# Optimization experiments

Hardware: AMD Instinct MI355X
Metric: run time of the kernel (lower is better)

The kernel has to match this reference:

```python
import jax, jax.numpy as jnp
import numpy as np

GRID = (52, 52)       # (grid_h, grid_w)
N_BOXES = 5
NORM = (416, 416)     # (norm_h, norm_w)
N_POLY = 4
IOU_THRESH = 0.4


def setup_inputs() -> dict:
    key = jax.random.key(0)
    x = jax.random.uniform(
        key, (1, GRID[0], GRID[1], N_BOXES * (N_POLY + 1)), dtype=jnp.float32)
    return {"x": x}


def _decode_coord(coord):
    # coord: [1, gh, gw, n_boxes, 4] -> decoded xyxy boxes [1, gh, gw, n_boxes, 4]
    gh, gw = GRID
    off_y, off_x = jnp.mgrid[:gh, :gw]
    off_x = off_x[None, :, :, None].astype(jnp.float32)   # [1, gh, gw, 1]
    off_y = off_y[None, :, :, None].astype(jnp.float32)
    sx = NORM[1] / gw
    sy = NORM[0] / gh
    cx = (coord[..., 0] + off_x) * sx
    w = coord[..., 2] * sx
    cy = (coord[..., 1] + off_y) * sy
    h = coord[..., 3] * sy
    cy = NORM[0] - cy  # y-axis flip as in original
    return jnp.stack([cx - w / 2, cy - h / 2, cx + w / 2, cy + h / 2], axis=-1)


def _nms_keep(boxes, scores):
    # Greedy NMS identical to tf.image.non_max_suppression (max_output = N).
    # Returns boolean keep mask in ORIGINAL box order.
    N = boxes.shape[0]
    order = jnp.argsort(-scores)           # descending by score
    b = boxes[order]
    x1, y1, x2, y2 = b[:, 0], b[:, 1], b[:, 2], b[:, 3]
    area = jnp.maximum(x2 - x1, 0.0) * jnp.maximum(y2 - y1, 0.0)
    iw = jnp.maximum(jnp.minimum(x2[:, None], x2[None, :]) -
                     jnp.maximum(x1[:, None], x1[None, :]), 0.0)
    ih = jnp.maximum(jnp.minimum(y2[:, None], y2[None, :]) -
                     jnp.maximum(y1[:, None], y1[None, :]), 0.0)
    inter = iw * ih
    union = area[:, None] + area[None, :] - inter
    iou = jnp.where(union > 0, inter / jnp.maximum(union, 1e-12), 0.0)  # [N, N]
    idx = jnp.arange(N)

    def body(i, active):
        suppress = (iou[i] > IOU_THRESH) & (idx > i) & active[i]
        return active & ~suppress

    active = jax.lax.fori_loop(0, N, body, jnp.ones(N, dtype=bool))
    return jnp.zeros(N, dtype=bool).at[order].set(active)


def reference(x):
    gh, gw = GRID
    y = x.reshape(1, gh, gw, N_BOXES, N_POLY + 1)
    boxes = _decode_coord(y[..., :4]).reshape(-1, 4)   # [N, 4]
    scores = y[..., 4].reshape(-1)                     # [N]
    keep = _nms_keep(jax.lax.stop_gradient(boxes),
                     jax.lax.stop_gradient(scores))
    # gather_nd + scatter_nd back into zeros == masked scores
    nms_scores = jnp.where(keep, scores, 0.0)
    out = jnp.concatenate([boxes[None], nms_scores[None, :, None]], axis=-1)
    return out.reshape(1, -1, N_POLY + 1)
```

## Files before the change

kernel.cpp:

```cpp
#include <hip/hip_runtime.h>

#define GH 52
#define GW 52
#define NB 5
#define NCELL (GH*GW)
#define NBOX (NCELL*NB)
#define SCALE 8.0f
#define NORMY 416.0f
#define IOU_T 0.4f

#define TS 4
#define HS (TS+2)
#define TBOX (HS*HS*NB)
#define NTX (GW/TS)
#define NTY (GH/TS)

#define PW (GW+2)
#define PCELLS ((GH+2)*PW)

__global__ __launch_bounds__(192) void decode_adj_kernel(
        const float* __restrict__ x, float* __restrict__ out,
        unsigned long long* __restrict__ masks) {
    __shared__ float4 lbox[TBOX];
    __shared__ float  lsc[TBOX];
    int bx0 = (blockIdx.x % NTX) * TS;
    int by0 = (blockIdx.x / NTX) * TS;
    int t = threadIdx.x;

    if (t < TBOX) {
        int lcell = t / NB, b = t % NB;
        int lx = lcell % HS, ly = lcell / HS;
        int gx = bx0 + lx - 1, gy = by0 + ly - 1;
        float4 bb = make_float4(0.f, 0.f, 0.f, 0.f);
        float s = -1e30f;
        if (gx >= 0 && gx < GW && gy >= 0 && gy < GH) {
            const float* p = x + ((size_t)(gy * GW + gx) * NB + b) * 5;
            float c0 = p[0], c1 = p[1], c2 = p[2], c3 = p[3]; s = p[4];
            float cx = (c0 + (float)gx) * SCALE;
            float w  = c2 * SCALE;
            float cy = NORMY - (c1 + (float)gy) * SCALE;
            float h  = c3 * SCALE;
            bb = make_float4(cx - w * 0.5f, cy - h * 0.5f,
                             cx + w * 0.5f, cy + h * 0.5f);
        }
        lbox[t] = bb; lsc[t] = s;
    }
    __syncthreads();

    if (t < TS * TS * NB) {
        int lcell = t / NB, b = t % NB;
        int lxi = lcell % TS, lyi = lcell / TS;
        int gx = bx0 + lxi, gy = by0 + lyi;
        int lt = ((lyi + 1) * HS + (lxi + 1)) * NB + b;
        float4 bj = lbox[lt]; float sj = lsc[lt];
        int cell = gy * GW + gx;
        int j = cell * NB + b;
        float areaj = fmaxf(bj.z - bj.x, 0.f) * fmaxf(bj.w - bj.y, 0.f);
        unsigned long long m = 0ull;
        #pragma unroll
        for (int dy = -1; dy <= 1; ++dy)
        #pragma unroll
        for (int dx = -1; dx <= 1; ++dx)
        #pragma unroll
        for (int nb2 = 0; nb2 < NB; ++nb2) {
            int ln = ((lyi + 1 + dy) * HS + (lxi + 1 + dx)) * NB + nb2;
            int i = j + (dy * GW + dx) * NB + (nb2 - b);
            if (i == j) continue;
            float si = lsc[ln];
            bool earlier = (si > sj) || (si == sj && i < j);
            if (!earlier) continue;
            float4 bi = lbox[ln];
            float iw = fmaxf(fminf(bi.z, bj.z) - fmaxf(bi.x, bj.x), 0.f);
            float ih = fmaxf(fminf(bi.w, bj.w) - fmaxf(bi.y, bj.y), 0.f);
            float inter = iw * ih;
            float areai = fmaxf(bi.z - bi.x, 0.f) * fmaxf(bi.w - bi.y, 0.f);
            float uni = areai + areaj - inter;
            float iou = (uni > 0.f) ? inter / fmaxf(uni, 1e-12f) : 0.f;
            if (iou > IOU_T)
                m |= 1ull << ((dy + 1) * 15 + (dx + 1) * 5 + nb2);
        }
        masks[b * NCELL + cell] = m;
        out[j * 5 + 0] = bj.x; out[j * 5 + 1] = bj.y;
        out[j * 5 + 2] = bj.z; out[j * 5 + 3] = bj.w;
        out[j * 5 + 4] = sj;
    }
}

__global__ __launch_bounds__(1024) void nms_kernel(
        const unsigned long long* __restrict__ masks,
        float* __restrict__ out) {
    __shared__ unsigned char act_s[PCELLS];
    __shared__ unsigned int rowflag[3][GH + 2];
    int tid = threadIdx.x;

    unsigned long long cm[3][NB];
    bool own[3];
    #pragma unroll
    for (int k = 0; k < 3; ++k) {
        int ct = tid + k * 1024;
        own[k] = (ct < NCELL);
        #pragma unroll
        for (int b = 0; b < NB; ++b)
            cm[k][b] = own[k] ? masks[b * NCELL + ct] : 0ull;
    }

    for (int i = tid; i < PCELLS; i += 1024) act_s[i] = 0;
    if (tid < GH + 2) {
        rowflag[0][tid] = 0;
        rowflag[1][tid] = 0;
        rowflag[2][tid] = (tid >= 1 && tid <= GH) ? 1u : 0u;
    }
    __syncthreads();
    for (int i = tid; i < NCELL; i += 1024) {
        int gy = i / GW, gx = i % GW;
        act_s[(gy + 1) * PW + (gx + 1)] = 0x1F;
    }
    __syncthreads();

    volatile unsigned char* act = act_s;

    int pprev = 2, pcur = 0, pnext = 1;
    for (int pass = 0; pass < 256; ++pass) {
        if (tid < GH + 2) rowflag[pnext][tid] = 0;
        const unsigned int* prevf = rowflag[pprev];
        bool mych = false;
        #pragma unroll
        for (int k = 0; k < 3; ++k) {
            if (!own[k]) continue;
            int ct = tid + k * 1024;
            int gy = ct / GW, gx = ct % GW;
            if ((prevf[gy] | prevf[gy + 1] | prevf[gy + 2]) == 0u) continue;
            int p0 = gy * PW + gx;
            unsigned r0 = (unsigned)act[p0]          | ((unsigned)act[p0 + 1] << 5)
                        | ((unsigned)act[p0 + 2] << 10);
            unsigned r1 = (unsigned)act[p0 + PW]     | ((unsigned)act[p0 + PW + 1] << 5)
                        | ((unsigned)act[p0 + PW + 2] << 10);
            unsigned r2 = (unsigned)act[p0 + 2 * PW] | ((unsigned)act[p0 + 2 * PW + 1] << 5)
                        | ((unsigned)act[p0 + 2 * PW + 2] << 10);
            unsigned long long V = (unsigned long long)r0
                                 | ((unsigned long long)r1 << 15)
                                 | ((unsigned long long)r2 << 30);
            unsigned nb = 0;
            #pragma unroll
            for (int b = 0; b < NB; ++b)
                nb |= ((V & cm[k][b]) == 0ull ? 1u : 0u) << b;
            int pc = p0 + PW + 1;
            if ((unsigned char)nb != act[pc]) {
                act[pc] = (unsigned char)nb;
                atomicOr(&rowflag[pcur][gy + 1], 1u);
                mych = true;
            }
        }
        if (__syncthreads_count(mych ? 1 : 0) == 0) break;
        int t0 = pprev; pprev = pcur; pcur = pnext; pnext = t0;
    }

    #pragma unroll
    for (int k = 0; k < 3; ++k) {
        if (!own[k]) continue;
        int ct = tid + k * 1024;
        int gy = ct / GW, gx = ct % GW;
        unsigned bits = act_s[(gy + 1) * PW + (gx + 1)];
        #pragma unroll
        for (int b = 0; b < NB; ++b) {
            int j = ct * NB + b;
            if (!((bits >> b) & 1u)) out[j * 5 + 4] = 0.0f;
        }
    }
}

extern "C" void kernel_launch(void* const* d_in, const int* in_sizes, int n_in,
                              void* d_out, int out_size, void* d_ws, size_t ws_size,
                              hipStream_t stream) {
    const float* x = (const float*)d_in[0];
    float* out = (float*)d_out;

    unsigned long long* masks = (unsigned long long*)d_ws;

    decode_adj_kernel<<<NTX * NTY, 192, 0, stream>>>(x, out, masks);
    nms_kernel<<<1, 1024, 0, stream>>>(masks, out);
}
```

Baseline: 72.26 us.

## Assign four-cell horizontal strips per thread in NMS fixed-point kernel

```diff
diff --git a/kernel.cpp b/kernel.cpp
--- a/kernel.cpp
+++ b/kernel.cpp
@@ -15,8 +15,12 @@
 #define NTX (GW/TS)
 #define NTY (GH/TS)
 
-#define PW (GW+2)
-#define PCELLS ((GH+2)*PW)
+#define PW2 56
+#define PR  54
+#define PC2 (PR*PW2)
+#define NSTRIP 13
+#define NTHR (GH*NSTRIP)
+#define BLK 704
 
 __global__ __launch_bounds__(192) void decode_adj_kernel(
         const float* __restrict__ x, float* __restrict__ out,
@@ -86,85 +90,90 @@
     }
 }
 
-__global__ __launch_bounds__(1024) void nms_kernel(
+__global__ __launch_bounds__(BLK) void nms_kernel(
         const unsigned long long* __restrict__ masks,
         float* __restrict__ out) {
-    __shared__ unsigned char act_s[PCELLS];
-    __shared__ unsigned int rowflag[3][GH + 2];
+    __shared__ __align__(16) unsigned char act_s[PC2];
+    __shared__ unsigned int rowflag[3][PR];
     int tid = threadIdx.x;
+    bool wk = tid < NTHR;
+    int row = tid / NSTRIP;
+    int s   = tid - row * NSTRIP;
+    int gx0 = s * 4;
+    int cell0 = row * GW + gx0;
 
-    unsigned long long cm[3][NB];
-    bool own[3];
+    unsigned long long cm[4][NB];
     #pragma unroll
-    for (int k = 0; k < 3; ++k) {
-        int ct = tid + k * 1024;
-        own[k] = (ct < NCELL);
+    for (int c = 0; c < 4; ++c)
         #pragma unroll
         for (int b = 0; b < NB; ++b)
-            cm[k][b] = own[k] ? masks[b * NCELL + ct] : 0ull;
-    }
+            cm[c][b] = wk ? masks[b * NCELL + cell0 + c] : 0ull;
 
-    for (int i = tid; i < PCELLS; i += 1024) act_s[i] = 0;
-    if (tid < GH + 2) {
+    for (int i = tid; i < PC2; i += BLK) act_s[i] = 0;
+    if (tid < PR) {
         rowflag[0][tid] = 0;
         rowflag[1][tid] = 0;
         rowflag[2][tid] = (tid >= 1 && tid <= GH) ? 1u : 0u;
     }
     __syncthreads();
-    for (int i = tid; i < NCELL; i += 1024) {
-        int gy = i / GW, gx = i % GW;
-        act_s[(gy + 1) * PW + (gx + 1)] = 0x1F;
+    for (int i = tid; i < NCELL; i += BLK) {
+        int gy = i / GW, gxx = i - gy * GW;
+        act_s[(gy + 1) * PW2 + gxx + 1] = 0x1F;
     }
     __syncthreads();
 
-    volatile unsigned char* act = act_s;
+    int p0 = row * PW2 + gx0;
+    int pc = (row + 1) * PW2 + gx0 + 1;
 
     int pprev = 2, pcur = 0, pnext = 1;
     for (int pass = 0; pass < 256; ++pass) {
-        if (tid < GH + 2) rowflag[pnext][tid] = 0;
+        if (tid < PR) rowflag[pnext][tid] = 0;
         const unsigned int* prevf = rowflag[pprev];
         bool mych = false;
-        #pragma unroll
-        for (int k = 0; k < 3; ++k) {
-            if (!own[k]) continue;
-            int ct = tid + k * 1024;
-            int gy = ct / GW, gx = ct % GW;
-            if ((prevf[gy] | prevf[gy + 1] | prevf[gy + 2]) == 0u) continue;
-            int p0 = gy * PW + gx;
-            unsigned r0 = (unsigned)act[p0]          | ((unsigned)act[p0 + 1] << 5)
-                        | ((unsigned)act[p0 + 2] << 10);
-            unsigned r1 = (unsigned)act[p0 + PW]     | ((unsigned)act[p0 + PW + 1] << 5)
-                        | ((unsigned)act[p0 + PW + 2] << 10);
-            unsigned r2 = (unsigned)act[p0 + 2 * PW] | ((unsigned)act[p0 + 2 * PW + 1] << 5)
-                        | ((unsigned)act[p0 + 2 * PW + 2] << 10);
-            unsigned long long V = (unsigned long long)r0
-                                 | ((unsigned long long)r1 << 15)
-                                 | ((unsigned long long)r2 << 30);
-            unsigned nb = 0;
+        if (wk && (prevf[row] | prevf[row + 1] | prevf[row + 2]) != 0u) {
+            unsigned r[3];
             #pragma unroll
-            for (int b = 0; b < NB; ++b)
-                nb |= ((V & cm[k][b]) == 0ull ? 1u : 0u) << b;
-            int pc = p0 + PW + 1;
-            if ((unsigned char)nb != act[pc]) {
-                act[pc] = (unsigned char)nb;
-                atomicOr(&rowflag[pcur][gy + 1], 1u);
-                mych = true;
+            for (int k = 0; k < 3; ++k) {
+                int p = p0 + k * PW2;
+                unsigned lo = *(volatile unsigned int*)(act_s + p);
+                unsigned hi = *(volatile unsigned short*)(act_s + p + 4);
+                r[k] = (lo & 0x1F)
+                     | (((lo >> 8)  & 0x1F) << 5)
+                     | (((lo >> 16) & 0x1F) << 10)
+                     | (((lo >> 24) & 0x1F) << 15)
+                     | ((hi & 0x1F) << 20)
+                     | (((hi >> 8) & 0x1F) << 25);
+            }
+            #pragma unroll
+            for (int c = 0; c < 4; ++c) {
+                unsigned long long V =
+                      (unsigned long long)((r[0] >> (5 * c)) & 0x7FFF)
+                    | ((unsigned long long)((r[1] >> (5 * c)) & 0x7FFF) << 15)
+                    | ((unsigned long long)((r[2] >> (5 * c)) & 0x7FFF) << 30);
+                unsigned nb = 0;
+                #pragma unroll
+                for (int b = 0; b < NB; ++b)
+                    nb |= ((V & cm[c][b]) == 0ull ? 1u : 0u) << b;
+                volatile unsigned char* pa = act_s + pc + c;
+                if ((unsigned char)nb != *pa) {
+                    *pa = (unsigned char)nb;
+                    rowflag[pcur][row + 1] = 1u;
+                    mych = true;
+                }
             }
         }
         if (__syncthreads_count(mych ? 1 : 0) == 0) break;
         int t0 = pprev; pprev = pcur; pcur = pnext; pnext = t0;
     }
 
-    #pragma unroll
-    for (int k = 0; k < 3; ++k) {
-        if (!own[k]) continue;
-        int ct = tid + k * 1024;
-        int gy = ct / GW, gx = ct % GW;
-        unsigned bits = act_s[(gy + 1) * PW + (gx + 1)];
+    if (wk) {
         #pragma unroll
-        for (int b = 0; b < NB; ++b) {
-            int j = ct * NB + b;
-            if (!((bits >> b) & 1u)) out[j * 5 + 4] = 0.0f;
+        for (int c = 0; c < 4; ++c) {
+            unsigned bits = act_s[pc + c];
+            int j0 = (cell0 + c) * NB;
+            #pragma unroll
+            for (int b = 0; b < NB; ++b)
+                if (!((bits >> b) & 1u)) out[(j0 + b) * 5 + 4] = 0.0f;
         }
     }
 }
@@ -178,5 +187,5 @@
     unsigned long long* masks = (unsigned long long*)d_ws;
 
     decode_adj_kernel<<<NTX * NTY, 192, 0, stream>>>(x, out, masks);
-    nms_kernel<<<1, 1024, 0, stream>>>(masks, out);
+    nms_kernel<<<1, BLK, 0, stream>>>(masks, out);
 }
```

Measured after the change: 73.19 us. Within noise of the previous version (+1.3%).

## Process NMS in score bands with bucketed box lists and intra-band fixpoint

Applied to the files above, without the earlier changes.

```diff
diff --git a/kernel.cpp b/kernel.cpp
--- a/kernel.cpp
+++ b/kernel.cpp
@@ -15,8 +15,18 @@
 #define NTX (GW/TS)
 #define NTY (GH/TS)
 
-#define PW (GW+2)
-#define PCELLS ((GH+2)*PW)
+#define KB 16
+#define MASK45 ((1ull<<45)-1)
+#define PW 54
+#define PCELLS (PW*PW)
+#define FCAP 192
+#define NT 256
+
+__device__ __forceinline__ int band16(float s) {
+    int q = (int)(s * 16.0f);
+    q = q < 0 ? 0 : (q > 15 ? 15 : q);
+    return 15 - q;
+}
 
 __global__ __launch_bounds__(192) void decode_adj_kernel(
         const float* __restrict__ x, float* __restrict__ out,
@@ -55,6 +65,8 @@
         float4 bj = lbox[lt]; float sj = lsc[lt];
         int cell = gy * GW + gx;
         int j = cell * NB + b;
+        int bdj = band16(sj);
+        bool inb = false;
         float areaj = fmaxf(bj.z - bj.x, 0.f) * fmaxf(bj.w - bj.y, 0.f);
         unsigned long long m = 0ull;
         #pragma unroll
@@ -76,96 +88,142 @@
             float areai = fmaxf(bi.z - bi.x, 0.f) * fmaxf(bi.w - bi.y, 0.f);
             float uni = areai + areaj - inter;
             float iou = (uni > 0.f) ? inter / fmaxf(uni, 1e-12f) : 0.f;
-            if (iou > IOU_T)
+            if (iou > IOU_T) {
                 m |= 1ull << ((dy + 1) * 15 + (dx + 1) * 5 + nb2);
-        }
-        masks[b * NCELL + cell] = m;
+                if (band16(si) == bdj) inb = true;
+            }
+        }
+        masks[j] = m | ((unsigned long long)bdj << 45)
+                     | (inb ? (1ull << 63) : 0ull);
         out[j * 5 + 0] = bj.x; out[j * 5 + 1] = bj.y;
         out[j * 5 + 2] = bj.z; out[j * 5 + 3] = bj.w;
         out[j * 5 + 4] = sj;
     }
 }
 
-__global__ __launch_bounds__(1024) void nms_kernel(
+__device__ __forceinline__ bool eval_box(volatile unsigned* A, unsigned e,
+                                         unsigned long long m45) {
+    int p = e & 0xFFF, b = (e >> 12) & 7;
+    unsigned a00 = A[p - PW - 1], a01 = A[p - PW], a02 = A[p - PW + 1];
+    unsigned a10 = A[p - 1],      a11 = A[p],      a12 = A[p + 1];
+    unsigned a20 = A[p + PW - 1], a21 = A[p + PW], a22 = A[p + PW + 1];
+    unsigned long long V = (unsigned long long)(a00 | (a01 << 5) | (a02 << 10))
+        | ((unsigned long long)(a10 | (a11 << 5) | (a12 << 10)) << 15)
+        | ((unsigned long long)(a20 | (a21 << 5) | (a22 << 10)) << 30);
+    unsigned na = ((V & m45) == 0ull) ? 1u : 0u;
+    unsigned old = (a11 >> b) & 1u;
+    if (na != old) {
+        if (na) atomicOr((unsigned*)(A + p), 1u << b);
+        else    atomicAnd((unsigned*)(A + p), ~(1u << b));
+        return true;
+    }
+    return false;
+}
+
+__global__ __launch_bounds__(NT) void nms_kernel(
         const unsigned long long* __restrict__ masks,
         float* __restrict__ out) {
-    __shared__ unsigned char act_s[PCELLS];
-    __shared__ unsigned int rowflag[3][GH + 2];
-    int tid = threadIdx.x;
-
-    unsigned long long cm[3][NB];
-    bool own[3];
-    #pragma unroll
-    for (int k = 0; k < 3; ++k) {
-        int ct = tid + k * 1024;
-        own[k] = (ct < NCELL);
+    __shared__ unsigned act[PCELLS];
+    __shared__ unsigned list[NBOX];
+    __shared__ unsigned flist[KB * FCAP];
+    __shared__ unsigned hcnt[4][KB];
+    __shared__ unsigned hoff[4][KB];
+    __shared__ unsigned fcnt[KB];
+    __shared__ unsigned bstart[KB + 1];
+    int t = threadIdx.x;
+    int w = t >> 6, lane = t & 63;
+
+    if (t < 4 * KB) ((unsigned*)hcnt)[t] = 0;
+    if (t < KB) fcnt[t] = 0;
+    for (int i = t; i < PCELLS; i += NT) {
+        int py = i / PW, px = i - py * PW;
+        act[i] = (py >= 1 && py <= GH && px >= 1 && px <= GW) ? 0x1Fu : 0u;
+    }
+    __syncthreads();
+
+    for (int j = t; j < NBOX; j += NT) {
+        unsigned long long mm = masks[j];
+        if (mm & MASK45) atomicAdd(&hcnt[w][(int)((mm >> 45) & 15)], 1u);
+    }
+    __syncthreads();
+
+    if (t < 64) {
+        int bd = t >> 2, ww = t & 3;
+        unsigned v = hcnt[ww][bd];
+        unsigned acc = v;
+        #pragma unroll
+        for (int d = 1; d < 64; d <<= 1) {
+            unsigned o = __shfl_up(acc, d);
+            if (lane >= d) acc += o;
+        }
+        unsigned excl = acc - v;
+        hoff[ww][bd] = excl;
+        if (ww == 0) bstart[bd] = excl;
+        if (t == 63) bstart[KB] = acc;
+    }
+    __syncthreads();
+
+    for (int j = t; j < NBOX; j += NT) {
+        unsigned long long mm = masks[j];
+        if (!(mm & MASK45)) continue;
+        int bd = (int)((mm >> 45) & 15);
+        int cell = j / NB, b = j - cell * NB;
+        int gy = cell / GW, gx = cell - gy * GW;
+        unsigned e = (unsigned)((gy + 1) * PW + gx + 1)
+                   | ((unsigned)b << 12) | ((unsigned)j << 15);
+        unsigned pos = atomicAdd(&hoff[w][bd], 1u);
+        list[pos] = e;
+        if (mm >> 63) {
+            unsigned fp = atomicAdd(&fcnt[bd], 1u);
+            if (fp < FCAP) flist[bd * FCAP + fp] = e;
+        }
+    }
+    __syncthreads();
+
+    volatile unsigned* A = act;
+    for (int bd = 0; bd < KB; ++bd) {
+        int s0 = bstart[bd], s1 = bstart[bd + 1];
+        unsigned ee[8]; unsigned long long mv[8]; int ne = 0;
+        for (int k = s0 + t; k < s1 && ne < 8; k += NT) ee[ne++] = list[k];
+        for (int i = 0; i < ne; ++i) mv[i] = masks[ee[i] >> 15] & MASK45;
+        for (int i = 0; i < ne; ++i) eval_box(A, ee[i], mv[i]);
+        for (int k = s0 + t + 8 * NT; k < s1; k += NT) {
+            unsigned e = list[k];
+            eval_box(A, e, masks[e >> 15] & MASK45);
+        }
+        __syncthreads();
+        if (w == 0) {
+            int fn = fcnt[bd];
+            if (fn > FCAP) {
+                for (int rr = 0; rr < 1024; ++rr) {
+                    bool ch = false;
+                    for (int k = s0 + lane; k < s1; k += 64) {
+                        unsigned e = list[k];
+                        ch |= eval_box(A, e, masks[e >> 15] & MASK45);
+                    }
+                    if (!__any(ch)) break;
+                }
+            } else if (fn > 0) {
+                unsigned fe[3]; unsigned long long fm[3]; int nf = 0;
+                for (int k = lane; k < fn && nf < 3; k += 64)
+                    fe[nf++] = flist[bd * FCAP + k];
+                for (int i = 0; i < nf; ++i) fm[i] = masks[fe[i] >> 15] & MASK45;
+                for (int rr = 0; rr < 256; ++rr) {
+                    bool ch = false;
+                    for (int i = 0; i < nf; ++i) ch |= eval_box(A, fe[i], fm[i]);
+                    if (!__any(ch)) break;
+                }
+            }
+        }
+        __syncthreads();
+    }
+
+    for (int c = t; c < NCELL; c += NT) {
+        int gy = c / GW, gx = c - gy * GW;
+        unsigned bits = act[(gy + 1) * PW + gx + 1];
         #pragma unroll
         for (int b = 0; b < NB; ++b)
-            cm[k][b] = own[k] ? masks[b * NCELL + ct] : 0ull;
-    }
-
-    for (int i = tid; i < PCELLS; i += 1024) act_s[i] = 0;
-    if (tid < GH + 2) {
-        rowflag[0][tid] = 0;
-        rowflag[1][tid] = 0;
-        rowflag[2][tid] = (tid >= 1 && tid <= GH) ? 1u : 0u;
-    }
-    __syncthreads();
-    for (int i = tid; i < NCELL; i += 1024) {
-        int gy = i / GW, gx = i % GW;
-        act_s[(gy + 1) * PW + (gx + 1)] = 0x1F;
-    }
-    __syncthreads();
-
-    volatile unsigned char* act = act_s;
-
-    int pprev = 2, pcur = 0, pnext = 1;
-    for (int pass = 0; pass < 256; ++pass) {
-        if (tid < GH + 2) rowflag[pnext][tid] = 0;
-        const unsigned int* prevf = rowflag[pprev];
-        bool mych = false;
-        #pragma unroll
-        for (int k = 0; k < 3; ++k) {
-            if (!own[k]) continue;
-            int ct = tid + k * 1024;
-            int gy = ct / GW, gx = ct % GW;
-            if ((prevf[gy] | prevf[gy + 1] | prevf[gy + 2]) == 0u) continue;
-            int p0 = gy * PW + gx;
-            unsigned r0 = (unsigned)act[p0]          | ((unsigned)act[p0 + 1] << 5)
-                        | ((unsigned)act[p0 + 2] << 10);
-            unsigned r1 = (unsigned)act[p0 + PW]     | ((unsigned)act[p0 + PW + 1] << 5)
-                        | ((unsigned)act[p0 + PW + 2] << 10);
-            unsigned r2 = (unsigned)act[p0 + 2 * PW] | ((unsigned)act[p0 + 2 * PW + 1] << 5)
-                        | ((unsigned)act[p0 + 2 * PW + 2] << 10);
-            unsigned long long V = (unsigned long long)r0
-                                 | ((unsigned long long)r1 << 15)
-                                 | ((unsigned long long)r2 << 30);
-            unsigned nb = 0;
-            #pragma unroll
-            for (int b = 0; b < NB; ++b)
-                nb |= ((V & cm[k][b]) == 0ull ? 1u : 0u) << b;
-            int pc = p0 + PW + 1;
-            if ((unsigned char)nb != act[pc]) {
-                act[pc] = (unsigned char)nb;
-                atomicOr(&rowflag[pcur][gy + 1], 1u);
-                mych = true;
-            }
-        }
-        if (__syncthreads_count(mych ? 1 : 0) == 0) break;
-        int t0 = pprev; pprev = pcur; pcur = pnext; pnext = t0;
-    }
-
-    #pragma unroll
-    for (int k = 0; k < 3; ++k) {
-        if (!own[k]) continue;
-        int ct = tid + k * 1024;
-        int gy = ct / GW, gx = ct % GW;
-        unsigned bits = act_s[(gy + 1) * PW + (gx + 1)];
-        #pragma unroll
-        for (int b = 0; b < NB; ++b) {
-            int j = ct * NB + b;
-            if (!((bits >> b) & 1u)) out[j * 5 + 4] = 0.0f;
-        }
+            if (!((bits >> b) & 1u)) out[(c * NB + b) * 5 + 4] = 0.0f;
     }
 }
 
@@ -178,5 +236,5 @@
     unsigned long long* masks = (unsigned long long*)d_ws;
 
     decode_adj_kernel<<<NTX * NTY, 192, 0, stream>>>(x, out, masks);
-    nms_kernel<<<1, 1024, 0, stream>>>(masks, out);
-}
+    nms_kernel<<<1, NT, 0, stream>>>(masks, out);
+}
```

Measured after the change: 121.3 us. +67.9%, slower.
